# Kernel optimization log

Hardware: AMD Instinct MI355X
Metric: run time of the kernel (lower is better)

The kernel has to match this reference:

```python
import jax, jax.numpy as jnp
import numpy as np

WIN_SIZE = 11
SIGMA = 1.5
WEIGHTS = np.array([0.0448, 0.2856, 0.3001, 0.2363, 0.1333], dtype=np.float32)
K1, K2 = 0.01, 0.03
DATA_RANGE = 255.0
C1 = (K1 * DATA_RANGE) ** 2
C2 = (K2 * DATA_RANGE) ** 2
N_SCALES = 5


def _gauss1d():
    coords = np.arange(WIN_SIZE, dtype=np.float32) - WIN_SIZE // 2
    g = np.exp(-(coords ** 2) / (2.0 * SIGMA ** 2))
    g /= g.sum()
    return jnp.asarray(g, dtype=jnp.float32)


def _blur(x, g):
    # separable depthwise gaussian blur, VALID padding (matches pytorch_msssim)
    C = x.shape[1]
    wh = jnp.tile(g.reshape(1, 1, 1, WIN_SIZE), (C, 1, 1, 1))
    wv = jnp.tile(g.reshape(1, 1, WIN_SIZE, 1), (C, 1, 1, 1))
    dn = ('NCHW', 'OIHW', 'NCHW')
    x = jax.lax.conv_general_dilated(x, wh, (1, 1), 'VALID', dimension_numbers=dn, feature_group_count=C)
    x = jax.lax.conv_general_dilated(x, wv, (1, 1), 'VALID', dimension_numbers=dn, feature_group_count=C)
    return x


def _ssim(X, Y, g):
    mu1 = _blur(X, g)
    mu2 = _blur(Y, g)
    mu1_sq = mu1 * mu1
    mu2_sq = mu2 * mu2
    mu1_mu2 = mu1 * mu2
    sigma1_sq = _blur(X * X, g) - mu1_sq
    sigma2_sq = _blur(Y * Y, g) - mu2_sq
    sigma12 = _blur(X * Y, g) - mu1_mu2
    cs_map = (2.0 * sigma12 + C2) / (sigma1_sq + sigma2_sq + C2)
    ssim_map = ((2.0 * mu1_mu2 + C1) / (mu1_sq + mu2_sq + C1)) * cs_map
    return ssim_map.mean(axis=(2, 3)), cs_map.mean(axis=(2, 3))  # [B,C] each


def _avg_pool2(x):
    # avg_pool2d kernel=2 stride=2; H,W chosen even at every scale so padding=0
    return jax.lax.reduce_window(x, 0.0, jax.lax.add, (1, 1, 2, 2), (1, 1, 2, 2), 'VALID') / 4.0


def setup_inputs() -> dict:
    key = jax.random.key(0)
    k1, k2 = jax.random.split(key)
    shape = (32, 3, 384, 384)
    prediction = jax.random.uniform(k1, shape, dtype=jnp.float32) * DATA_RANGE
    truth = jax.random.uniform(k2, shape, dtype=jnp.float32) * DATA_RANGE
    return {"prediction": prediction, "truth": truth}


def reference(prediction, truth):
    g = _gauss1d()
    w = jnp.asarray(WEIGHTS)
    X, Y = prediction, truth
    mcs = []
    for i in range(N_SCALES):
        ssim_pc, cs = _ssim(X, Y, g)
        if i < N_SCALES - 1:
            mcs.append(jax.nn.relu(cs))
            X = _avg_pool2(X)
            Y = _avg_pool2(Y)
    vals = jnp.stack(mcs + [jax.nn.relu(ssim_pc)], axis=0)  # [5,B,C]
    ms_ssim_val = jnp.prod(vals ** w.reshape(-1, 1, 1), axis=0)  # [B,C]
    return 1.0 - ms_ssim_val.mean()
```

## Files before the change

### kernel.cpp

```cpp
#include <hip/hip_runtime.h>
#include <math.h>


namespace {

constexpr int NIMG = 96;
constexpr float TWO_C1 = 13.005f;
constexpr float TWO_C2 = 117.045f;

__device__ constexpr float GW[11] = {
    0.00102838f, 0.00759875f, 0.03600077f, 0.10936070f, 0.21300553f,
    0.26601172f,
    0.21300553f, 0.10936070f, 0.03600077f, 0.00759875f, 0.00102838f};

typedef float f2 __attribute__((ext_vector_type(2)));

__device__ __forceinline__ void pk_fma(f2& d, f2 a, f2 b) {
  asm("v_pk_fma_f32 %0, %1, %2, %0" : "+v"(d) : "v"(a), "v"(b));
}
__device__ __forceinline__ f2 pk_mul(f2 a, f2 b) {
  f2 d;
  asm("v_pk_mul_f32 %0, %1, %2" : "=v"(d) : "v"(a), "v"(b));
  return d;
}

__device__ __forceinline__ float wshl1(float v) {
  return __int_as_float(__builtin_amdgcn_mov_dpp(
      __float_as_int(v), 0x130, 0xF, 0xF, true));
}
__device__ __forceinline__ f2 wshl1v(f2 v) {
  f2 r;
  r.x = wshl1(v.x);
  r.y = wshl1(v.y);
  return r;
}

struct SPtrs {
  const float* x[5];
  const float* y[5];
};

template <bool BASE>
__device__ __forceinline__ void tap(int j, float a, float b, f2 (&A)[16],
                                    f2 (&B)[16], const f2 (&wtv)[11]) {
  f2 P;
  if (BASE) { P.x = a + b; P.y = a - b; }
  else      { P.x = a;     P.y = b;     }
  f2 Q = pk_mul(P, P);
#pragma unroll
  for (int i = 0; i < 16; ++i) {
    const int k = j - i;
    if (k >= 0 && k <= 10) {
      pk_fma(A[i], wtv[k], P);
      pk_fma(B[i], wtv[k], Q);
    }
  }
}

template <bool BASE, bool CLAMP>
__device__ __forceinline__ void vblur(const float* __restrict__ Xi,
                                      const float* __restrict__ Yi, int row0,
                                      int W, int H, int cin, f2 (&A)[16],
                                      f2 (&B)[16], const f2 (&wtv)[11]) {
#pragma unroll
  for (int j = 0; j < 26; ++j) {
    int rin = row0 + j;
    if (CLAMP) rin = rin < H - 1 ? rin : H - 1;
    float a = Xi[(size_t)rin * W + cin];
    float b = Yi[(size_t)rin * W + cin];
    tap<BASE>(j, a, b, A, B, wtv);
  }
}

__global__ __launch_bounds__(256) void ssim_all(SPtrs sp,
                                                float* __restrict__ acc) {
  __shared__ float red[2][4];

  const int tile = blockIdx.x;
  int s;
  if (tile < 42) s = 0;
  else if (tile < 54) s = 1;
  else if (tile < 58) s = 2;
  else if (tile < 59) s = 3;
  else s = 4;
  const int tstart[5] = {0, 42, 54, 58, 59};
  const int HH[5] = {384, 192, 96, 48, 24};
  const int TXc[5] = {7, 4, 2, 1, 1};
  const int lt = tile - tstart[s];
  const int H = HH[s], W = H, OH = H - 10, OW = W - 10;
  const int tx = lt % TXc[s], ty = lt / TXc[s];
  const int img = blockIdx.z;
  const float* Xi = sp.x[s] + (size_t)img * H * W;
  const float* Yi = sp.y[s] + (size_t)img * H * W;
  const bool base = (s == 0);

  const int t = threadIdx.x;
  const int lane = t & 63, wv = t >> 6;
  const int col = tx * 54 + lane;
  const int cin = col < W - 1 ? col : W - 1;
  const int row0 = ty * 64 + wv * 16;

  f2 wtv[11];
#pragma unroll
  for (int k = 0; k < 11; ++k) { wtv[k].x = GW[k]; wtv[k].y = GW[k]; }

  float ssim_s = 0.f, cs_s = 0.f;

  if (row0 < OH) {
    f2 A[16] = {}, B[16] = {};
    const bool noclamp = (row0 + 25 <= H - 1);
    if (base) {
      if (noclamp) vblur<true, false>(Xi, Yi, row0, W, H, cin, A, B, wtv);
      else         vblur<true, true >(Xi, Yi, row0, W, H, cin, A, B, wtv);
    } else {
      if (noclamp) vblur<false, false>(Xi, Yi, row0, W, H, cin, A, B, wtv);
      else         vblur<false, true >(Xi, Yi, row0, W, H, cin, A, B, wtv);
    }

    const bool colok = (lane < 54) && (col < OW);
#pragma unroll
    for (int i = 0; i < 16; ++i) {
      f2 tA = A[i], tB = B[i];
      f2 bA = pk_mul(wtv[0], tA);
      f2 bB = pk_mul(wtv[0], tB);
#pragma unroll
      for (int k = 1; k <= 10; ++k) {
        tA = wshl1v(tA); pk_fma(bA, wtv[k], tA);
        tB = wshl1v(tB); pk_fma(bB, wtv[k], tB);
      }
      if (colok && (row0 + i < OH)) {
        float m2u = bA.x * bA.x, m2w = bA.y * bA.y;
        float Pm = m2u - m2w;
        float Qm = m2u + m2w;
        float Am = bB.x - bB.y;
        float Bm = bB.x + bB.y;
        float cs = (Am - Pm + TWO_C2) *
                   __builtin_amdgcn_rcpf(Bm - Qm + TWO_C2);
        float l = (Pm + TWO_C1) * __builtin_amdgcn_rcpf(Qm + TWO_C1);
        cs_s += cs;
        ssim_s += l * cs;
      }
    }
  }

#pragma unroll
  for (int off = 32; off > 0; off >>= 1) {
    ssim_s += __shfl_down(ssim_s, off);
    cs_s += __shfl_down(cs_s, off);
  }
  if (lane == 0) { red[0][wv] = ssim_s; red[1][wv] = cs_s; }
  __syncthreads();
  if (t == 0) {
    atomicAdd(&acc[(2 * s + 0) * NIMG + img],
              red[0][0] + red[0][1] + red[0][2] + red[0][3]);
    atomicAdd(&acc[(2 * s + 1) * NIMG + img],
              red[1][0] + red[1][1] + red[1][2] + red[1][3]);
  }
}

__global__ __launch_bounds__(256) void pyramid_kernel(
    const float* __restrict__ X, const float* __restrict__ Y,
    float* __restrict__ u1, float* __restrict__ w1,
    float* __restrict__ u2, float* __restrict__ w2,
    float* __restrict__ u3, float* __restrict__ w3,
    float* __restrict__ u4, float* __restrict__ w4,
    float* __restrict__ acc) {
  const int img = blockIdx.y;
  const int t = threadIdx.x;
  if (blockIdx.x == 0 && img == 0) {
    for (int i = t; i < 10 * NIMG; i += 256) acc[i] = 0.f;
  }
  const int wv = t >> 6, lane = t & 63;
  const int tidx = blockIdx.x * 4 + wv;
  const int tx = tidx % 24, ty = tidx / 24;
  const int r = lane >> 3, c = lane & 7;

  const float* Xs = X + (size_t)img * 384 * 384;
  const float* Ys = Y + (size_t)img * 384 * 384;
  float* o1[2] = {u1 + (size_t)img * 192 * 192, w1 + (size_t)img * 192 * 192};
  float* o2[2] = {u2 + (size_t)img * 96 * 96,   w2 + (size_t)img * 96 * 96};
  float* o3[2] = {u3 + (size_t)img * 48 * 48,   w3 + (size_t)img * 48 * 48};
  float* o4[2] = {u4 + (size_t)img * 24 * 24,   w4 + (size_t)img * 24 * 24};

  int gr = ty * 16 + 2 * r, gc = tx * 16 + 2 * c;
  float2 xu = *(const float2*)&Xs[(size_t)gr * 384 + gc];
  float2 xv = *(const float2*)&Xs[(size_t)(gr + 1) * 384 + gc];
  float2 yu = *(const float2*)&Ys[(size_t)gr * 384 + gc];
  float2 yv = *(const float2*)&Ys[(size_t)(gr + 1) * 384 + gc];
  float l1x = 0.25f * (xu.x + xu.y + xv.x + xv.y);
  float l1y = 0.25f * (yu.x + yu.y + yv.x + yv.y);
  float lv[2] = {l1x + l1y, l1x - l1y};

#pragma unroll
  for (int ch = 0; ch < 2; ++ch) {
    float l1 = lv[ch];
    o1[ch][(size_t)(ty * 8 + r) * 192 + tx * 8 + c] = l1;

    float l2 = l1 + __shfl_xor(l1, 1);
    l2 = 0.25f * (l2 + __shfl_xor(l2, 8));
    if ((r & 1) == 0 && (c & 1) == 0)
      o2[ch][(size_t)(ty * 4 + (r >> 1)) * 96 + tx * 4 + (c >> 1)] = l2;

    float l3 = l2 + __shfl_xor(l2, 2);
    l3 = 0.25f * (l3 + __shfl_xor(l3, 16));
    if ((r & 3) == 0 && (c & 3) == 0)
      o3[ch][(size_t)(ty * 2 + (r >> 2)) * 48 + tx * 2 + (c >> 2)] = l3;

    float l4 = l3 + __shfl_xor(l3, 4);
    l4 = 0.25f * (l4 + __shfl_xor(l4, 32));
    if (lane == 0) o4[ch][(size_t)ty * 24 + tx] = l4;
  }
}

__global__ void final_kernel(const float* __restrict__ acc,
                             float* __restrict__ out) {
  __shared__ float prods[NIMG];
  const float wts[5] = {0.0448f, 0.2856f, 0.3001f, 0.2363f, 0.1333f};
  const float inv_npix[5] = {1.f / (374.f * 374.f), 1.f / (182.f * 182.f),
                             1.f / (86.f * 86.f),  1.f / (38.f * 38.f),
                             1.f / (14.f * 14.f)};
  int t = threadIdx.x;
  if (t < NIMG) {
    float p = 1.f;
#pragma unroll
    for (int s = 0; s < 5; ++s) {
      float sum = (s < 4) ? acc[(s * 2 + 1) * NIMG + t]
                          : acc[(s * 2 + 0) * NIMG + t];
      float m = sum * inv_npix[s];
      m = m > 0.f ? m : 0.f;
      p *= powf(m, wts[s]);
    }
    prods[t] = p;
  }
  __syncthreads();
  if (t == 0) {
    float s = 0.f;
    for (int i = 0; i < NIMG; ++i) s += prods[i];
    out[0] = 1.f - s / (float)NIMG;
  }
}

}

extern "C" void kernel_launch(void* const* d_in, const int* in_sizes, int n_in,
                              void* d_out, int out_size, void* d_ws,
                              size_t ws_size, hipStream_t stream) {
  const float* X0 = (const float*)d_in[0];
  const float* Y0 = (const float*)d_in[1];
  float* out = (float*)d_out;
  float* ws = (float*)d_ws;

  const size_t L1 = (size_t)NIMG * 192 * 192;
  const size_t L2 = (size_t)NIMG * 96 * 96;
  const size_t L3 = (size_t)NIMG * 48 * 48;
  const size_t L4 = (size_t)NIMG * 24 * 24;

  float* u1 = ws;
  float* u2 = u1 + L1;
  float* u3 = u2 + L2;
  float* u4 = u3 + L3;
  float* w1 = u4 + L4;
  float* w2 = w1 + L1;
  float* w3 = w2 + L2;
  float* w4 = w3 + L3;
  float* acc = w4 + L4;

  pyramid_kernel<<<dim3(144, NIMG), dim3(256), 0, stream>>>(
      X0, Y0, u1, w1, u2, w2, u3, w3, u4, w4, acc);

  SPtrs sp;
  sp.x[0] = X0; sp.x[1] = u1; sp.x[2] = u2; sp.x[3] = u3; sp.x[4] = u4;
  sp.y[0] = Y0; sp.y[1] = w1; sp.y[2] = w2; sp.y[3] = w3; sp.y[4] = w4;

  ssim_all<<<dim3(60, 1, NIMG), dim3(256), 0, stream>>>(sp, acc);

  final_kernel<<<dim3(1), dim3(128), 0, stream>>>(acc, out);
}
```

Measured before the change: 238.9 us.

## Process two columns per lane with packed float2 loads and symmetric-weight horizontal blur

Each lane now loads a float2 and handles two adjacent output columns, so a wave covers about 128 columns instead of 54. Tiles shrink to 8 rows per wave and 32 rows per block, and the grid is retiled. The horizontal blur uses op_sel packed FMAs with paired symmetric Gaussian weights, which halves the DPP shifts per output. The aim is fewer redundant halo loads and fewer shift and FMA instructions per pixel. The cost is more vertical halo overhead per row (18 loads for 8 rows instead of 26 for 16) and reliance on hand-written op_sel inline assembly.

```diff
diff --git a/kernel.cpp b/kernel.cpp
--- a/kernel.cpp
+++ b/kernel.cpp
@@ -15,13 +15,36 @@
 
 typedef float f2 __attribute__((ext_vector_type(2)));
 
-__device__ __forceinline__ void pk_fma(f2& d, f2 a, f2 b) {
-  asm("v_pk_fma_f32 %0, %1, %2, %0" : "+v"(d) : "v"(a), "v"(b));
-}
 __device__ __forceinline__ f2 pk_mul(f2 a, f2 b) {
   f2 d;
   asm("v_pk_mul_f32 %0, %1, %2" : "=v"(d) : "v"(a), "v"(b));
   return d;
+}
+__device__ __forceinline__ f2 pk_mul_s1lo(f2 a, f2 b) {
+  f2 d;
+  asm("v_pk_mul_f32 %0, %1, %2 op_sel:[0,0] op_sel_hi:[1,0]"
+      : "=v"(d) : "v"(a), "v"(b));
+  return d;
+}
+__device__ __forceinline__ void fma_w(f2& d, f2 q, f2 p) {
+  asm("v_pk_fma_f32 %0, %1, %2, %0 op_sel:[0,0,0] op_sel_hi:[0,1,1]"
+      : "+v"(d) : "v"(q), "v"(p));
+}
+__device__ __forceinline__ void fma_nl(f2& d, f2 q, f2 t) {
+  asm("v_pk_fma_f32 %0, %1, %2, %0 op_sel:[0,0,0] op_sel_hi:[1,0,1]"
+      : "+v"(d) : "v"(q), "v"(t));
+}
+__device__ __forceinline__ void fma_nh(f2& d, f2 q, f2 t) {
+  asm("v_pk_fma_f32 %0, %1, %2, %0 op_sel:[0,1,0] op_sel_hi:[1,1,1]"
+      : "+v"(d) : "v"(q), "v"(t));
+}
+__device__ __forceinline__ void fma_sl(f2& d, f2 q, f2 t) {
+  asm("v_pk_fma_f32 %0, %1, %2, %0 op_sel:[1,0,0] op_sel_hi:[0,0,1]"
+      : "+v"(d) : "v"(q), "v"(t));
+}
+__device__ __forceinline__ void fma_sh(f2& d, f2 q, f2 t) {
+  asm("v_pk_fma_f32 %0, %1, %2, %0 op_sel:[1,1,0] op_sel_hi:[0,1,1]"
+      : "+v"(d) : "v"(q), "v"(t));
 }
 
 __device__ __forceinline__ float wshl1(float v) {
@@ -40,105 +63,125 @@
   const float* y[5];
 };
 
-template <bool BASE>
-__device__ __forceinline__ void tap(int j, float a, float b, f2 (&A)[16],
-                                    f2 (&B)[16], const f2 (&wtv)[11]) {
-  f2 P;
-  if (BASE) { P.x = a + b; P.y = a - b; }
-  else      { P.x = a;     P.y = b;     }
-  f2 Q = pk_mul(P, P);
-#pragma unroll
-  for (int i = 0; i < 16; ++i) {
-    const int k = j - i;
-    if (k >= 0 && k <= 10) {
-      pk_fma(A[i], wtv[k], P);
-      pk_fma(B[i], wtv[k], Q);
-    }
-  }
-}
-
 template <bool BASE, bool CLAMP>
-__device__ __forceinline__ void vblur(const float* __restrict__ Xi,
-                                      const float* __restrict__ Yi, int row0,
-                                      int W, int H, int cin, f2 (&A)[16],
-                                      f2 (&B)[16], const f2 (&wtv)[11]) {
-#pragma unroll
-  for (int j = 0; j < 26; ++j) {
+__device__ __forceinline__ void vblur(const f2* __restrict__ PA,
+                                      const f2* __restrict__ PB, int row0,
+                                      int W2, int H, int cp, f2 (&AU)[8],
+                                      f2 (&AW)[8], f2 (&BU)[8], f2 (&BW)[8],
+                                      const f2 (&QQ)[6]) {
+#pragma unroll
+  for (int j = 0; j < 18; ++j) {
     int rin = row0 + j;
     if (CLAMP) rin = rin < H - 1 ? rin : H - 1;
-    float a = Xi[(size_t)rin * W + cin];
-    float b = Yi[(size_t)rin * W + cin];
-    tap<BASE>(j, a, b, A, B, wtv);
-  }
-}
-
-__global__ __launch_bounds__(256) void ssim_all(SPtrs sp,
-                                                float* __restrict__ acc) {
+    f2 pa = PA[(size_t)rin * W2 + cp];
+    f2 pb = PB[(size_t)rin * W2 + cp];
+    f2 Pu, Pw;
+    if (BASE) { Pu = pa + pb; Pw = pa - pb; }
+    else      { Pu = pa;      Pw = pb;      }
+    f2 Qu = pk_mul(Pu, Pu), Qw = pk_mul(Pw, Pw);
+#pragma unroll
+    for (int i = 0; i < 8; ++i) {
+      const int k = j - i;
+      if (k >= 0 && k <= 10) {
+        const int qi = k <= 5 ? k : 10 - k;
+        fma_w(AU[i], QQ[qi], Pu);
+        fma_w(AW[i], QQ[qi], Pw);
+        fma_w(BU[i], QQ[qi], Qu);
+        fma_w(BW[i], QQ[qi], Qw);
+      }
+    }
+  }
+}
+
+__global__ __launch_bounds__(256, 4) void ssim_all(SPtrs sp,
+                                                   float* __restrict__ acc) {
   __shared__ float red[2][4];
 
   const int tile = blockIdx.x;
   int s;
-  if (tile < 42) s = 0;
-  else if (tile < 54) s = 1;
-  else if (tile < 58) s = 2;
-  else if (tile < 59) s = 3;
+  if (tile < 48) s = 0;
+  else if (tile < 60) s = 1;
+  else if (tile < 63) s = 2;
+  else if (tile < 65) s = 3;
   else s = 4;
-  const int tstart[5] = {0, 42, 54, 58, 59};
+  const int tstart[5] = {0, 48, 60, 63, 65};
   const int HH[5] = {384, 192, 96, 48, 24};
-  const int TXc[5] = {7, 4, 2, 1, 1};
+  const int NTX[5] = {4, 2, 1, 1, 1};
+  const int TWM[5] = {94, 92, 86, 38, 14};
   const int lt = tile - tstart[s];
-  const int H = HH[s], W = H, OH = H - 10, OW = W - 10;
-  const int tx = lt % TXc[s], ty = lt / TXc[s];
+  const int H = HH[s], W = H, OH = H - 10, OW = W - 10, W2 = W >> 1;
+  const int tx = lt % NTX[s], by = lt / NTX[s];
+  const int x0 = tx * TWM[s];
+  const int tw = (TWM[s] < OW - x0) ? TWM[s] : OW - x0;
   const int img = blockIdx.z;
-  const float* Xi = sp.x[s] + (size_t)img * H * W;
-  const float* Yi = sp.y[s] + (size_t)img * H * W;
-  const bool base = (s == 0);
+  const f2* PA = (const f2*)sp.x[s] + (size_t)img * H * W2;
+  const f2* PB = (const f2*)sp.y[s] + (size_t)img * H * W2;
 
   const int t = threadIdx.x;
   const int lane = t & 63, wv = t >> 6;
-  const int col = tx * 54 + lane;
-  const int cin = col < W - 1 ? col : W - 1;
-  const int row0 = ty * 64 + wv * 16;
-
-  f2 wtv[11];
-#pragma unroll
-  for (int k = 0; k < 11; ++k) { wtv[k].x = GW[k]; wtv[k].y = GW[k]; }
+  int cp = (x0 >> 1) + lane;
+  cp = cp < W2 - 1 ? cp : W2 - 1;
+  const int row0 = by * 32 + wv * 8;
+
+  f2 QQ[6];
+  QQ[0].x = GW[0]; QQ[0].y = 0.f;
+#pragma unroll
+  for (int n = 1; n < 6; ++n) { QQ[n].x = GW[n]; QQ[n].y = GW[n - 1]; }
 
   float ssim_s = 0.f, cs_s = 0.f;
 
   if (row0 < OH) {
-    f2 A[16] = {}, B[16] = {};
-    const bool noclamp = (row0 + 25 <= H - 1);
-    if (base) {
-      if (noclamp) vblur<true, false>(Xi, Yi, row0, W, H, cin, A, B, wtv);
-      else         vblur<true, true >(Xi, Yi, row0, W, H, cin, A, B, wtv);
+    f2 AU[8] = {}, AW[8] = {}, BU[8] = {}, BW[8] = {};
+    const bool noclamp = (row0 + 17 <= H - 1);
+    if (s == 0) {
+      if (noclamp) vblur<true, false>(PA, PB, row0, W2, H, cp, AU, AW, BU, BW, QQ);
+      else         vblur<true, true >(PA, PB, row0, W2, H, cp, AU, AW, BU, BW, QQ);
     } else {
-      if (noclamp) vblur<false, false>(Xi, Yi, row0, W, H, cin, A, B, wtv);
-      else         vblur<false, true >(Xi, Yi, row0, W, H, cin, A, B, wtv);
+      if (noclamp) vblur<false, false>(PA, PB, row0, W2, H, cp, AU, AW, BU, BW, QQ);
+      else         vblur<false, true >(PA, PB, row0, W2, H, cp, AU, AW, BU, BW, QQ);
     }
 
-    const bool colok = (lane < 54) && (col < OW);
-#pragma unroll
-    for (int i = 0; i < 16; ++i) {
-      f2 tA = A[i], tB = B[i];
-      f2 bA = pk_mul(wtv[0], tA);
-      f2 bB = pk_mul(wtv[0], tB);
-#pragma unroll
-      for (int k = 1; k <= 10; ++k) {
-        tA = wshl1v(tA); pk_fma(bA, wtv[k], tA);
-        tB = wshl1v(tB); pk_fma(bB, wtv[k], tB);
-      }
-      if (colok && (row0 + i < OH)) {
-        float m2u = bA.x * bA.x, m2w = bA.y * bA.y;
-        float Pm = m2u - m2w;
-        float Qm = m2u + m2w;
-        float Am = bB.x - bB.y;
-        float Bm = bB.x + bB.y;
-        float cs = (Am - Pm + TWO_C2) *
-                   __builtin_amdgcn_rcpf(Bm - Qm + TWO_C2);
-        float l = (Pm + TWO_C1) * __builtin_amdgcn_rcpf(Qm + TWO_C1);
-        cs_s += cs;
-        ssim_s += l * cs;
+    auto hb = [&QQ](f2 tt) -> f2 {
+      f2 h = pk_mul_s1lo(QQ[0], tt);
+      fma_nh(h, QQ[1], tt);
+      tt = wshl1v(tt);
+      fma_nl(h, QQ[2], tt);
+      fma_nh(h, QQ[3], tt);
+      tt = wshl1v(tt);
+      fma_nl(h, QQ[4], tt);
+      fma_nh(h, QQ[5], tt);
+      tt = wshl1v(tt);
+      fma_sl(h, QQ[5], tt);
+      fma_sh(h, QQ[4], tt);
+      tt = wshl1v(tt);
+      fma_sl(h, QQ[3], tt);
+      fma_sh(h, QQ[2], tt);
+      tt = wshl1v(tt);
+      fma_sl(h, QQ[1], tt);
+      fma_sh(h, QQ[0], tt);
+      return h;
+    };
+
+    const bool vx = (2 * lane) < tw;
+    const bool vy = (2 * lane + 1) < tw;
+#pragma unroll
+    for (int i = 0; i < 8; ++i) {
+      if (row0 + i < OH) {
+        f2 bU = hb(AU[i]), bW = hb(AW[i]);
+        f2 bU2 = hb(BU[i]), bW2 = hb(BW[i]);
+        f2 m2u = pk_mul(bU, bU), m2w = pk_mul(bW, bW);
+        f2 Pm = m2u - m2w;
+        f2 Qm = m2u + m2w;
+        f2 Am = bU2 - bW2;
+        f2 Bm = bU2 + bW2;
+        float csx = (Am.x - Pm.x + TWO_C2) *
+                    __builtin_amdgcn_rcpf(Bm.x - Qm.x + TWO_C2);
+        float lx = (Pm.x + TWO_C1) * __builtin_amdgcn_rcpf(Qm.x + TWO_C1);
+        float csy = (Am.y - Pm.y + TWO_C2) *
+                    __builtin_amdgcn_rcpf(Bm.y - Qm.y + TWO_C2);
+        float ly = (Pm.y + TWO_C1) * __builtin_amdgcn_rcpf(Qm.y + TWO_C1);
+        if (vx) { cs_s += csx; ssim_s += lx * csx; }
+        if (vy) { cs_s += csy; ssim_s += ly * csy; }
       }
     }
   }
@@ -272,7 +315,7 @@
   sp.x[0] = X0; sp.x[1] = u1; sp.x[2] = u2; sp.x[3] = u3; sp.x[4] = u4;
   sp.y[0] = Y0; sp.y[1] = w1; sp.y[2] = w2; sp.y[3] = w3; sp.y[4] = w4;
 
-  ssim_all<<<dim3(60, 1, NIMG), dim3(256), 0, stream>>>(sp, acc);
+  ssim_all<<<dim3(66, 1, NIMG), dim3(256), 0, stream>>>(sp, acc);
 
   final_kernel<<<dim3(1), dim3(128), 0, stream>>>(acc, out);
 }
```

New measurement: 238.8 us. No clear change (-0.0%).
